# Optimization experiments

Measured on AMD Instinct MI355X. Metric: run time of the kernel, lower is better.

## Reference

```python
import jax, jax.numpy as jnp
import numpy as np

B, E, H, A = 16384, 128, 256, 20


def _xavier(key, shape):
    scale = (2.0 / (shape[0] + shape[1])) ** 0.5
    return (jax.random.normal(key, shape, jnp.float32) * scale).astype(jnp.float32)


def setup_inputs() -> dict:
    key = jax.random.key(0)
    ks = jax.random.split(key, 16)
    d = {
        'x1': jax.random.normal(ks[0], (B, E), jnp.float32),
        'x2': jax.random.normal(ks[1], (B, A, E), jnp.float32),
        'h': jax.random.normal(ks[2], (B, H), jnp.float32),
        'c1': jax.random.normal(ks[3], (B, H), jnp.float32),
        'c2': jax.random.normal(ks[4], (B, H), jnp.float32),
    }
    gate_names = ['f', 'i', 'c', 'o']
    for j, n in enumerate(gate_names):
        d[f'W1_{n}'] = _xavier(ks[5 + 2 * j], (H + E, H))
        d[f'W2_{n}'] = _xavier(ks[6 + 2 * j], (H + E, H))
        d[f'b1_{n}'] = jnp.zeros((H,), jnp.float32)
        d[f'b2_{n}'] = jnp.zeros((H,), jnp.float32)
    d['W_attn'] = _xavier(ks[13], (H + 2 * E, 1))
    return d


def reference(x1, x2, h, c1, c2,
              W1_f, W2_f, b1_f, b2_f,
              W1_i, W2_i, b1_i, b2_i,
              W1_c, W2_c, b1_c, b2_c,
              W1_o, W2_o, b1_o, b2_o,
              W_attn):
    hx1 = jnp.concatenate([h, x1], axis=1)                    # [B, H+E]
    # attention: score_a = [h, x1, x2_a] @ W_attn ; split W_attn to vectorize
    base = hx1 @ W_attn[:H + E, 0]                            # [B]
    scores = base[:, None] + jnp.einsum('bae,e->ba', x2, W_attn[H + E:, 0])  # [B, A]
    attn = jax.nn.softmax(scores, axis=1)
    x2m = jnp.einsum('ba,bae->be', attn, x2)                  # [B, E]
    hx2 = jnp.concatenate([h, x2m], axis=1)                   # [B, H+E]

    f1 = jax.nn.sigmoid(hx1 @ W1_f + b1_f)
    f2 = jax.nn.sigmoid(hx2 @ W2_f + b2_f)
    i1 = jax.nn.sigmoid(hx1 @ W1_i + b1_i)
    i2 = jax.nn.sigmoid(hx2 @ W2_i + b2_i)
    c1t = jnp.tanh(hx1 @ W1_c + b1_c)
    c2t = jnp.tanh(hx2 @ W2_c + b2_c)
    c1n = f1 * c1 + i1 * c1t
    c2n = f2 * c2 + i2 * c2t

    o1 = hx1 @ W1_o + b1_o
    o2 = hx2 @ W2_o + b2_o
    # exp(o1)/(exp(o1)+exp(o2)) mixing == softmax over the 2-cell axis (stable form)
    g = jax.nn.softmax(jnp.stack([o1, o2], axis=0), axis=0)
    h_new = g[0] * jnp.tanh(c1n) + g[1] * jnp.tanh(c2n)
    return (h_new, c1n, c2n)
```

## Files before the change

kernel.cpp:

```cpp
#include <hip/hip_runtime.h>
#include <hip/hip_bf16.h>

#define B_SZ 16384
#define E_SZ 128
#define H_SZ 256
#define A_SZ 20
#define K_SZ 384
#define BH   (B_SZ * H_SZ)

typedef __attribute__((ext_vector_type(8))) short  short8v;
typedef __attribute__((ext_vector_type(4))) float  f32x4;
typedef __attribute__((ext_vector_type(2))) float  f32x2;
typedef __attribute__((ext_vector_type(4))) unsigned short ushort4v;
typedef __attribute__((ext_vector_type(2))) unsigned short ushort2v;

__device__ __forceinline__ unsigned short f2bf(float f) {
    union { float f; unsigned u; } v; v.f = f;
    unsigned r = v.u + 0x7fffu + ((v.u >> 16) & 1u);
    return (unsigned short)(r >> 16);
}

__device__ __forceinline__ float wsum(float v) {
    #pragma unroll
    for (int off = 32; off > 0; off >>= 1) v += __shfl_xor(v, off, 64);
    return v;
}

__device__ __forceinline__ float sigm(float x) { return 1.0f / (1.0f + __expf(-x)); }

struct Ptr8 { const float* p[8]; };

__global__ __launch_bounds__(256) void attn_pack(
    const float* __restrict__ x1, const float* __restrict__ x2,
    const float* __restrict__ h,  const float* __restrict__ wa,
    unsigned short* __restrict__ A1, unsigned short* __restrict__ A2)
{
    const int row  = blockIdx.x * 4 + (threadIdx.x >> 6);
    const int lane = threadIdx.x & 63;

    const f32x4 hv   = *(const f32x4*)(h  + (size_t)row * H_SZ + 4 * lane);
    const f32x2 x1v  = *(const f32x2*)(x1 + (size_t)row * E_SZ + 2 * lane);
    const f32x4 wah  = *(const f32x4*)(wa + 4 * lane);
    const f32x2 wax1 = *(const f32x2*)(wa + H_SZ + 2 * lane);
    const f32x2 wax2 = *(const f32x2*)(wa + H_SZ + E_SZ + 2 * lane);

    float base = hv.x * wah.x + hv.y * wah.y + hv.z * wah.z + hv.w * wah.w
               + x1v.x * wax1.x + x1v.y * wax1.y;

    f32x2 xv[A_SZ];
    float sp[A_SZ];
    const float* x2r = x2 + (size_t)row * A_SZ * E_SZ;
    #pragma unroll
    for (int a = 0; a < A_SZ; ++a) {
        xv[a] = *(const f32x2*)(x2r + a * E_SZ + 2 * lane);
        sp[a] = xv[a].x * wax2.x + xv[a].y * wax2.y;
    }

    base = wsum(base);
    #pragma unroll
    for (int a = 0; a < A_SZ; ++a) sp[a] = wsum(sp[a]) + base;

    float mx = sp[0];
    #pragma unroll
    for (int a = 1; a < A_SZ; ++a) mx = fmaxf(mx, sp[a]);
    float s = 0.0f;
    #pragma unroll
    for (int a = 0; a < A_SZ; ++a) { sp[a] = __expf(sp[a] - mx); s += sp[a]; }
    const float inv = 1.0f / s;

    float m0 = 0.0f, m1 = 0.0f;
    #pragma unroll
    for (int a = 0; a < A_SZ; ++a) { m0 += sp[a] * xv[a].x; m1 += sp[a] * xv[a].y; }
    m0 *= inv; m1 *= inv;

    ushort4v hb;
    hb.x = f2bf(hv.x); hb.y = f2bf(hv.y); hb.z = f2bf(hv.z); hb.w = f2bf(hv.w);
    *(ushort4v*)(A1 + (size_t)row * K_SZ + 4 * lane) = hb;
    *(ushort4v*)(A2 + (size_t)row * K_SZ + 4 * lane) = hb;
    ushort2v x1b; x1b.x = f2bf(x1v.x); x1b.y = f2bf(x1v.y);
    *(ushort2v*)(A1 + (size_t)row * K_SZ + H_SZ + 2 * lane) = x1b;
    ushort2v mb; mb.x = f2bf(m0); mb.y = f2bf(m1);
    *(ushort2v*)(A2 + (size_t)row * K_SZ + H_SZ + 2 * lane) = mb;
}

__global__ __launch_bounds__(256) void pack_w(Ptr8 ws, unsigned short* __restrict__ Wt)
{
    const int g = blockIdx.z, nt = blockIdx.y, kt = blockIdx.x;
    __shared__ float tile[64][65];
    const float* W = ws.p[g];
    const int c = threadIdx.x & 63, r0 = threadIdx.x >> 6;
    #pragma unroll
    for (int i = 0; i < 16; ++i) {
        int r = r0 + 4 * i;
        tile[r][c] = W[(size_t)(kt * 64 + r) * H_SZ + nt * 64 + c];
    }
    __syncthreads();
    #pragma unroll
    for (int i = 0; i < 16; ++i) {
        int rr = r0 + 4 * i;
        const int hcol = nt * 64 + rr;
        const int nn = ((hcol >> 5) << 8) + g * 32 + (hcol & 31);
        Wt[(size_t)nn * K_SZ + kt * 64 + c] = f2bf(tile[c][rr]);
    }
}

__global__ __launch_bounds__(512, 1) void gemm_ep(
    const unsigned short* __restrict__ A1, const unsigned short* __restrict__ A2,
    const unsigned short* __restrict__ Wt, Ptr8 bias,
    const float* __restrict__ c1, const float* __restrict__ c2,
    float* __restrict__ out)
{
    __shared__ char smem[131072];
    const int tid = threadIdx.x, w = tid >> 6, lane = tid & 63;
    const int d = blockIdx.x;
    const int rb  = (d & 7) * 16 + (d >> 6);
    const int hcb = (d >> 3) & 7;
    const int row0 = rb * 128, hcol0 = hcb * 32;
    const int fr = lane & 15, hi = lane >> 4;
    const int wM = w >> 2, wN = w & 3;

    const unsigned short* Bpan = Wt + (size_t)hcb * 256 * K_SZ;
    const int Rl = tid >> 3, sl = tid & 7;

    auto stage = [&](int buf, int ks) {
        const int bufb = buf * 65536;
        #pragma unroll
        for (int i = 0; i < 2; ++i) {
            const int R = i * 64 + Rl;
            const unsigned short* src =
                A1 + (size_t)(row0 + R) * K_SZ + ks * 64 + ((sl ^ (R & 7)) << 3);
            __builtin_amdgcn_global_load_lds(
                (const __attribute__((address_space(1))) unsigned int*)src,
                (__attribute__((address_space(3))) unsigned int*)
                    (smem + bufb + i * 8192 + w * 1024), 16, 0, 0);
        }
        #pragma unroll
        for (int i = 0; i < 2; ++i) {
            const int R = i * 64 + Rl;
            const unsigned short* src =
                A2 + (size_t)(row0 + R) * K_SZ + ks * 64 + ((sl ^ (R & 7)) << 3);
            __builtin_amdgcn_global_load_lds(
                (const __attribute__((address_space(1))) unsigned int*)src,
                (__attribute__((address_space(3))) unsigned int*)
                    (smem + bufb + 16384 + i * 8192 + w * 1024), 16, 0, 0);
        }
        #pragma unroll
        for (int j = 0; j < 4; ++j) {
            const int C = j * 64 + Rl;
            const unsigned short* src =
                Bpan + (size_t)C * K_SZ + ks * 64 + ((sl ^ (C & 7)) << 3);
            __builtin_amdgcn_global_load_lds(
                (const __attribute__((address_space(1))) unsigned int*)src,
                (__attribute__((address_space(3))) unsigned int*)
                    (smem + bufb + 32768 + j * 8192 + w * 1024), 16, 0, 0);
        }
    };

    f32x4 acc[4][4];
    #pragma unroll
    for (int mi = 0; mi < 4; ++mi)
        #pragma unroll
        for (int ni = 0; ni < 4; ++ni) acc[mi][ni] = (f32x4){0.f, 0.f, 0.f, 0.f};

    const int apan = (wN >= 2) ? 16384 : 0;

    stage(0, 0);
    int buf = 0;
    for (int ks = 0; ks < 6; ++ks) {
        __syncthreads();
        if (ks < 5) stage(buf ^ 1, ks + 1);
        const char* bb = smem + buf * 65536;
        #pragma unroll
        for (int kk = 0; kk < 2; ++kk) {
            short8v af[4], bf[4];
            #pragma unroll
            for (int mi = 0; mi < 4; ++mi) {
                const int R = wM * 64 + mi * 16 + fr;
                af[mi] = *(const short8v*)(bb + apan + R * 128 +
                                           ((((kk << 2) + hi) ^ (R & 7)) << 4));
            }
            #pragma unroll
            for (int ni = 0; ni < 4; ++ni) {
                const int C = wN * 64 + ni * 16 + fr;
                bf[ni] = *(const short8v*)(bb + 32768 + C * 128 +
                                           ((((kk << 2) + hi) ^ (C & 7)) << 4));
            }
            #pragma unroll
            for (int mi = 0; mi < 4; ++mi)
                #pragma unroll
                for (int ni = 0; ni < 4; ++ni)
                    acc[mi][ni] = __builtin_amdgcn_mfma_f32_16x16x32_bf16(
                        af[mi], bf[ni], acc[mi][ni], 0, 0, 0);
        }
        buf ^= 1;
    }

    const int hcin = tid & 31, rsl = tid >> 5;
    float c1p[8], c2p[8], bia[8];
    #pragma unroll
    for (int rr = 0; rr < 8; ++rr) {
        const int R = rsl * 8 + rr;
        c1p[rr] = c1[(size_t)(row0 + R) * H_SZ + hcol0 + hcin];
        c2p[rr] = c2[(size_t)(row0 + R) * H_SZ + hcol0 + hcin];
    }
    #pragma unroll
    for (int g = 0; g < 8; ++g) bia[g] = bias.p[g][hcol0 + hcin];

    __syncthreads();
    float* gf = (float*)smem;
    #pragma unroll
    for (int mi = 0; mi < 4; ++mi)
        #pragma unroll
        for (int ni = 0; ni < 4; ++ni)
            #pragma unroll
            for (int j = 0; j < 4; ++j) {
                const int R  = wM * 64 + mi * 16 + hi * 4 + j;
                const int g  = wN * 2 + (ni >> 1);
                const int hc = (ni & 1) * 16 + fr;
                const int hcr = (hc + ((R >> 2) & 3) * 8) & 31;
                gf[g * 4096 + R * 32 + hcr] = acc[mi][ni][j];
            }
    __syncthreads();

    #pragma unroll
    for (int rr = 0; rr < 8; ++rr) {
        const int R = rsl * 8 + rr;
        const int hcr = (hcin + ((R >> 2) & 3) * 8) & 31;
        float G[8];
        #pragma unroll
        for (int g = 0; g < 8; ++g) G[g] = gf[g * 4096 + R * 32 + hcr] + bia[g];

        const float f1  = sigm(G[0]);
        const float i1  = sigm(G[1]);
        const float c1t = tanhf(G[2]);
        const float o1  = G[3];
        const float f2  = sigm(G[4]);
        const float i2  = sigm(G[5]);
        const float c2t = tanhf(G[6]);
        const float o2  = G[7];
        const float c1n = f1 * c1p[rr] + i1 * c1t;
        const float c2n = f2 * c2p[rr] + i2 * c2t;
        const float mo  = fmaxf(o1, o2);
        const float e1  = __expf(o1 - mo), e2 = __expf(o2 - mo);
        const float g0  = e1 / (e1 + e2);
        const float hn  = g0 * tanhf(c1n) + (1.0f - g0) * tanhf(c2n);

        const size_t o0 = (size_t)(row0 + R) * H_SZ + hcol0 + hcin;
        out[o0]          = hn;
        out[BH + o0]     = c1n;
        out[2 * BH + o0] = c2n;
    }
}

extern "C" void kernel_launch(void* const* d_in, const int* in_sizes, int n_in,
                              void* d_out, int out_size, void* d_ws, size_t ws_size,
                              hipStream_t stream)
{
    const float* x1 = (const float*)d_in[0];
    const float* x2 = (const float*)d_in[1];
    const float* h  = (const float*)d_in[2];
    const float* c1 = (const float*)d_in[3];
    const float* c2 = (const float*)d_in[4];
    const float* wa = (const float*)d_in[21];

    Ptr8 wptr, bptr;
    wptr.p[0] = (const float*)d_in[5];  wptr.p[1] = (const float*)d_in[9];
    wptr.p[2] = (const float*)d_in[13]; wptr.p[3] = (const float*)d_in[17];
    wptr.p[4] = (const float*)d_in[6];  wptr.p[5] = (const float*)d_in[10];
    wptr.p[6] = (const float*)d_in[14]; wptr.p[7] = (const float*)d_in[18];
    bptr.p[0] = (const float*)d_in[7];  bptr.p[1] = (const float*)d_in[11];
    bptr.p[2] = (const float*)d_in[15]; bptr.p[3] = (const float*)d_in[19];
    bptr.p[4] = (const float*)d_in[8];  bptr.p[5] = (const float*)d_in[12];
    bptr.p[6] = (const float*)d_in[16]; bptr.p[7] = (const float*)d_in[20];

    char* ws = (char*)d_ws;
    unsigned short* A1 = (unsigned short*)(ws);
    unsigned short* A2 = (unsigned short*)(ws + 12582912);
    unsigned short* Wt = (unsigned short*)(ws + 25165824);

    pack_w<<<dim3(6, 4, 8), 256, 0, stream>>>(wptr, Wt);
    attn_pack<<<B_SZ / 4, 256, 0, stream>>>(x1, x2, h, wa, A1, A2);
    gemm_ep<<<1024, 512, 0, stream>>>(A1, A2, Wt, bptr, c1, c2, (float*)d_out);
}
```

Baseline: 108.1 us.

## Share bf16 h panel across cells, single-buffer LDS to raise GEMM occupancy

The packed A operands are split into a shared bf16 h array plus separate x1 and attention-mixed x2 arrays. This removes the duplicated h write and lets the GEMM load the h k-slices once for both cells instead of twice. The GEMM drops double buffering and halves LDS to 64KB, targeting several blocks per CU under a launch bound of 4. The epilogue is done in two 64-row passes and c1/c2 are prefetched before the main loop. The cost is that global-to-LDS loads no longer overlap MFMA within a block, with latency hiding left to other resident blocks.

Result: slower. 125.5 us (+16.1%).

```diff
diff --git a/kernel.cpp b/kernel.cpp
--- a/kernel.cpp
+++ b/kernel.cpp
@@ -33,7 +33,8 @@
 __global__ __launch_bounds__(256) void attn_pack(
     const float* __restrict__ x1, const float* __restrict__ x2,
     const float* __restrict__ h,  const float* __restrict__ wa,
-    unsigned short* __restrict__ A1, unsigned short* __restrict__ A2)
+    unsigned short* __restrict__ Hb, unsigned short* __restrict__ A1x,
+    unsigned short* __restrict__ A2x)
 {
     const int row  = blockIdx.x * 4 + (threadIdx.x >> 6);
     const int lane = threadIdx.x & 63;
@@ -75,12 +76,11 @@
 
     ushort4v hb;
     hb.x = f2bf(hv.x); hb.y = f2bf(hv.y); hb.z = f2bf(hv.z); hb.w = f2bf(hv.w);
-    *(ushort4v*)(A1 + (size_t)row * K_SZ + 4 * lane) = hb;
-    *(ushort4v*)(A2 + (size_t)row * K_SZ + 4 * lane) = hb;
+    *(ushort4v*)(Hb + (size_t)row * H_SZ + 4 * lane) = hb;
     ushort2v x1b; x1b.x = f2bf(x1v.x); x1b.y = f2bf(x1v.y);
-    *(ushort2v*)(A1 + (size_t)row * K_SZ + H_SZ + 2 * lane) = x1b;
+    *(ushort2v*)(A1x + (size_t)row * E_SZ + 2 * lane) = x1b;
     ushort2v mb; mb.x = f2bf(m0); mb.y = f2bf(m1);
-    *(ushort2v*)(A2 + (size_t)row * K_SZ + H_SZ + 2 * lane) = mb;
+    *(ushort2v*)(A2x + (size_t)row * E_SZ + 2 * lane) = mb;
 }
 
 __global__ __launch_bounds__(256) void pack_w(Ptr8 ws, unsigned short* __restrict__ Wt)
@@ -104,13 +104,13 @@
     }
 }
 
-__global__ __launch_bounds__(512, 1) void gemm_ep(
-    const unsigned short* __restrict__ A1, const unsigned short* __restrict__ A2,
-    const unsigned short* __restrict__ Wt, Ptr8 bias,
-    const float* __restrict__ c1, const float* __restrict__ c2,
+__global__ __launch_bounds__(512, 4) void gemm_ep(
+    const unsigned short* __restrict__ Hb, const unsigned short* __restrict__ A1x,
+    const unsigned short* __restrict__ A2x, const unsigned short* __restrict__ Wt,
+    Ptr8 bias, const float* __restrict__ c1, const float* __restrict__ c2,
     float* __restrict__ out)
 {
-    __shared__ char smem[131072];
+    __shared__ char smem[65536];
     const int tid = threadIdx.x, w = tid >> 6, lane = tid & 63;
     const int d = blockIdx.x;
     const int rb  = (d & 7) * 16 + (d >> 6);
@@ -120,39 +120,49 @@
     const int wM = w >> 2, wN = w & 3;
 
     const unsigned short* Bpan = Wt + (size_t)hcb * 256 * K_SZ;
-    const int Rl = tid >> 3, sl = tid & 7;
-
-    auto stage = [&](int buf, int ks) {
-        const int bufb = buf * 65536;
-        #pragma unroll
-        for (int i = 0; i < 2; ++i) {
-            const int R = i * 64 + Rl;
-            const unsigned short* src =
-                A1 + (size_t)(row0 + R) * K_SZ + ks * 64 + ((sl ^ (R & 7)) << 3);
-            __builtin_amdgcn_global_load_lds(
-                (const __attribute__((address_space(1))) unsigned int*)src,
-                (__attribute__((address_space(3))) unsigned int*)
-                    (smem + bufb + i * 8192 + w * 1024), 16, 0, 0);
-        }
-        #pragma unroll
-        for (int i = 0; i < 2; ++i) {
-            const int R = i * 64 + Rl;
-            const unsigned short* src =
-                A2 + (size_t)(row0 + R) * K_SZ + ks * 64 + ((sl ^ (R & 7)) << 3);
-            __builtin_amdgcn_global_load_lds(
-                (const __attribute__((address_space(1))) unsigned int*)src,
-                (__attribute__((address_space(3))) unsigned int*)
-                    (smem + bufb + 16384 + i * 8192 + w * 1024), 16, 0, 0);
-        }
+    const int lr = lane >> 3, sl = lane & 7;
+
+    const int hcin = tid & 31, rgrp = tid >> 5;
+    float c1p[2][4], c2p[2][4], bia[8];
+    #pragma unroll
+    for (int p = 0; p < 2; ++p)
+        #pragma unroll
+        for (int rr = 0; rr < 4; ++rr) {
+            const int R = p * 64 + rgrp * 4 + rr;
+            c1p[p][rr] = c1[(size_t)(row0 + R) * H_SZ + hcol0 + hcin];
+            c2p[p][rr] = c2[(size_t)(row0 + R) * H_SZ + hcol0 + hcin];
+        }
+    #pragma unroll
+    for (int g = 0; g < 8; ++g) bia[g] = bias.p[g][hcol0 + hcin];
+
+    auto glds = [&](const unsigned short* src, int dstoff) {
+        __builtin_amdgcn_global_load_lds(
+            (const __attribute__((address_space(1))) unsigned int*)src,
+            (__attribute__((address_space(3))) unsigned int*)(smem + dstoff), 16, 0, 0);
+    };
+    auto stage = [&](int ks) {
         #pragma unroll
         for (int j = 0; j < 4; ++j) {
-            const int C = j * 64 + Rl;
-            const unsigned short* src =
-                Bpan + (size_t)C * K_SZ + ks * 64 + ((sl ^ (C & 7)) << 3);
-            __builtin_amdgcn_global_load_lds(
-                (const __attribute__((address_space(1))) unsigned int*)src,
-                (__attribute__((address_space(3))) unsigned int*)
-                    (smem + bufb + 32768 + j * 8192 + w * 1024), 16, 0, 0);
+            const int C = j * 64 + w * 8 + lr;
+            glds(Bpan + (size_t)C * K_SZ + ks * 64 + ((sl ^ (C & 7)) << 3),
+                 32768 + j * 8192 + w * 1024);
+        }
+        if (ks < 4) {
+            #pragma unroll
+            for (int i = 0; i < 2; ++i) {
+                const int R = i * 64 + w * 8 + lr;
+                glds(Hb + (size_t)(row0 + R) * H_SZ + ks * 64 + ((sl ^ (R & 7)) << 3),
+                     i * 8192 + w * 1024);
+            }
+        } else {
+            const int ko = (ks - 4) * 64;
+            #pragma unroll
+            for (int i = 0; i < 2; ++i) {
+                const int R = i * 64 + w * 8 + lr;
+                const int sw = (sl ^ (R & 7)) << 3;
+                glds(A1x + (size_t)(row0 + R) * E_SZ + ko + sw,         i * 8192 + w * 1024);
+                glds(A2x + (size_t)(row0 + R) * E_SZ + ko + sw, 16384 + i * 8192 + w * 1024);
+            }
         }
     };
 
@@ -162,27 +172,23 @@
         #pragma unroll
         for (int ni = 0; ni < 4; ++ni) acc[mi][ni] = (f32x4){0.f, 0.f, 0.f, 0.f};
 
-    const int apan = (wN >= 2) ? 16384 : 0;
-
-    stage(0, 0);
-    int buf = 0;
+    stage(0);
     for (int ks = 0; ks < 6; ++ks) {
         __syncthreads();
-        if (ks < 5) stage(buf ^ 1, ks + 1);
-        const char* bb = smem + buf * 65536;
+        const int apo = (ks >= 4 && wN >= 2) ? 16384 : 0;
         #pragma unroll
         for (int kk = 0; kk < 2; ++kk) {
             short8v af[4], bf[4];
             #pragma unroll
             for (int mi = 0; mi < 4; ++mi) {
                 const int R = wM * 64 + mi * 16 + fr;
-                af[mi] = *(const short8v*)(bb + apan + R * 128 +
+                af[mi] = *(const short8v*)(smem + apo + R * 128 +
                                            ((((kk << 2) + hi) ^ (R & 7)) << 4));
             }
             #pragma unroll
             for (int ni = 0; ni < 4; ++ni) {
                 const int C = wN * 64 + ni * 16 + fr;
-                bf[ni] = *(const short8v*)(bb + 32768 + C * 128 +
+                bf[ni] = *(const short8v*)(smem + 32768 + C * 128 +
                                            ((((kk << 2) + hi) ^ (C & 7)) << 4));
             }
             #pragma unroll
@@ -192,63 +198,57 @@
                     acc[mi][ni] = __builtin_amdgcn_mfma_f32_16x16x32_bf16(
                         af[mi], bf[ni], acc[mi][ni], 0, 0, 0);
         }
-        buf ^= 1;
-    }
-
-    const int hcin = tid & 31, rsl = tid >> 5;
-    float c1p[8], c2p[8], bia[8];
-    #pragma unroll
-    for (int rr = 0; rr < 8; ++rr) {
-        const int R = rsl * 8 + rr;
-        c1p[rr] = c1[(size_t)(row0 + R) * H_SZ + hcol0 + hcin];
-        c2p[rr] = c2[(size_t)(row0 + R) * H_SZ + hcol0 + hcin];
-    }
-    #pragma unroll
-    for (int g = 0; g < 8; ++g) bia[g] = bias.p[g][hcol0 + hcin];
-
-    __syncthreads();
+        __syncthreads();
+        if (ks < 5) stage(ks + 1);
+    }
+
     float* gf = (float*)smem;
     #pragma unroll
-    for (int mi = 0; mi < 4; ++mi)
-        #pragma unroll
-        for (int ni = 0; ni < 4; ++ni)
-            #pragma unroll
-            for (int j = 0; j < 4; ++j) {
-                const int R  = wM * 64 + mi * 16 + hi * 4 + j;
-                const int g  = wN * 2 + (ni >> 1);
-                const int hc = (ni & 1) * 16 + fr;
-                const int hcr = (hc + ((R >> 2) & 3) * 8) & 31;
-                gf[g * 4096 + R * 32 + hcr] = acc[mi][ni][j];
-            }
-    __syncthreads();
-
-    #pragma unroll
-    for (int rr = 0; rr < 8; ++rr) {
-        const int R = rsl * 8 + rr;
-        const int hcr = (hcin + ((R >> 2) & 3) * 8) & 31;
-        float G[8];
-        #pragma unroll
-        for (int g = 0; g < 8; ++g) G[g] = gf[g * 4096 + R * 32 + hcr] + bia[g];
-
-        const float f1  = sigm(G[0]);
-        const float i1  = sigm(G[1]);
-        const float c1t = tanhf(G[2]);
-        const float o1  = G[3];
-        const float f2  = sigm(G[4]);
-        const float i2  = sigm(G[5]);
-        const float c2t = tanhf(G[6]);
-        const float o2  = G[7];
-        const float c1n = f1 * c1p[rr] + i1 * c1t;
-        const float c2n = f2 * c2p[rr] + i2 * c2t;
-        const float mo  = fmaxf(o1, o2);
-        const float e1  = __expf(o1 - mo), e2 = __expf(o2 - mo);
-        const float g0  = e1 / (e1 + e2);
-        const float hn  = g0 * tanhf(c1n) + (1.0f - g0) * tanhf(c2n);
-
-        const size_t o0 = (size_t)(row0 + R) * H_SZ + hcol0 + hcin;
-        out[o0]          = hn;
-        out[BH + o0]     = c1n;
-        out[2 * BH + o0] = c2n;
+    for (int p = 0; p < 2; ++p) {
+        __syncthreads();
+        if (wM == p) {
+            #pragma unroll
+            for (int mi = 0; mi < 4; ++mi)
+                #pragma unroll
+                for (int ni = 0; ni < 4; ++ni)
+                    #pragma unroll
+                    for (int j = 0; j < 4; ++j) {
+                        const int Rl2 = mi * 16 + hi * 4 + j;
+                        const int g   = wN * 2 + (ni >> 1);
+                        const int hc  = (ni & 1) * 16 + fr;
+                        const int hcr = (hc + (((Rl2 >> 2) & 1) << 4)) & 31;
+                        gf[(g * 64 + Rl2) * 32 + hcr] = acc[mi][ni][j];
+                    }
+        }
+        __syncthreads();
+        #pragma unroll
+        for (int rr = 0; rr < 4; ++rr) {
+            const int Rl2 = rgrp * 4 + rr;
+            const int hcr = (hcin + (((Rl2 >> 2) & 1) << 4)) & 31;
+            float G[8];
+            #pragma unroll
+            for (int g = 0; g < 8; ++g) G[g] = gf[(g * 64 + Rl2) * 32 + hcr] + bia[g];
+
+            const float f1  = sigm(G[0]);
+            const float i1  = sigm(G[1]);
+            const float c1t = tanhf(G[2]);
+            const float o1  = G[3];
+            const float f2  = sigm(G[4]);
+            const float i2  = sigm(G[5]);
+            const float c2t = tanhf(G[6]);
+            const float o2  = G[7];
+            const float c1n = f1 * c1p[p][rr] + i1 * c1t;
+            const float c2n = f2 * c2p[p][rr] + i2 * c2t;
+            const float mo  = fmaxf(o1, o2);
+            const float e1  = __expf(o1 - mo), e2 = __expf(o2 - mo);
+            const float g0  = e1 / (e1 + e2);
+            const float hn  = g0 * tanhf(c1n) + (1.0f - g0) * tanhf(c2n);
+
+            const size_t o0 = (size_t)(row0 + p * 64 + Rl2) * H_SZ + hcol0 + hcin;
+            out[o0]          = hn;
+            out[BH + o0]     = c1n;
+            out[2 * BH + o0] = c2n;
+        }
     }
 }
 
@@ -274,11 +274,12 @@
     bptr.p[6] = (const float*)d_in[16]; bptr.p[7] = (const float*)d_in[20];
 
     char* ws = (char*)d_ws;
-    unsigned short* A1 = (unsigned short*)(ws);
-    unsigned short* A2 = (unsigned short*)(ws + 12582912);
-    unsigned short* Wt = (unsigned short*)(ws + 25165824);
+    unsigned short* Hb  = (unsigned short*)(ws);
+    unsigned short* A1x = (unsigned short*)(ws + 8388608);
+    unsigned short* A2x = (unsigned short*)(ws + 12582912);
+    unsigned short* Wt  = (unsigned short*)(ws + 16777216);
 
     pack_w<<<dim3(6, 4, 8), 256, 0, stream>>>(wptr, Wt);
-    attn_pack<<<B_SZ / 4, 256, 0, stream>>>(x1, x2, h, wa, A1, A2);
-    gemm_ep<<<1024, 512, 0, stream>>>(A1, A2, Wt, bptr, c1, c2, (float*)d_out);
-}
+    attn_pack<<<B_SZ / 4, 256, 0, stream>>>(x1, x2, h, wa, Hb, A1x, A2x);
+    gemm_ep<<<1024, 512, 0, stream>>>(Hb, A1x, A2x, Wt, bptr, c1, c2, (float*)d_out);
+}
```
